# Kernel tuning notes

Measured on AMD Instinct MI355X. Metric: run time of the kernel, lower is better.

The kernel has to match this reference:

```python
import jax, jax.numpy as jnp
import numpy as np

N, D, T = 8192, 512, 65536


def setup_inputs() -> dict:
    key = jax.random.key(0)
    kx, kt = jax.random.split(key)
    x = jax.random.normal(kx, (N, D), dtype=jnp.float32)
    triplets = jax.random.randint(kt, (T, 3), 0, N, dtype=jnp.int64)
    return {"x": x, "triplets": triplets}


def reference(x, triplets):
    # Gather anchor/positive/negative rows instead of building the full NxN
    # distance matrix the torch code materializes; math is identical since
    # dist[i,j] = ||x[i]-x[j]||^2 (clamped at 0, which direct computation guarantees).
    i, j, k = triplets[:, 0], triplets[:, 1], triplets[:, 2]
    xi, xj, xk = x[i], x[j], x[k]          # [T, D] each
    d_ij = jnp.sum((xi - xj) ** 2, axis=-1)  # [T]
    d_ik = jnp.sum((xi - xk) ** 2, axis=-1)  # [T]
    # loss = mean over triplets of log(1 + exp(d_ij - d_ik))
    loss = jnp.mean(jax.nn.softplus(d_ij - d_ik))
    return loss.reshape(1)
```

## Files before the change

### kernel.cpp

```cpp
#include <hip/hip_runtime.h>
#include <hip/hip_fp16.h>


typedef float floatx2 __attribute__((ext_vector_type(2)));

#define NTRIP  65536
#define DIM    512
#define NROWS  8192
#define NSLICE 32
#define SLICE_U4 NROWS
#define GGRP   8
#define TRIP_PER_G (NTRIP / GGRP)
#define BT     1024
#define NIT    (TRIP_PER_G / BT)
#define NSLOT  64
#define SLOT_STRIDE 16

#define XQS_BYTES ((size_t)NSLICE * SLICE_U4 * 16)
#define ZP_BYTES  ((size_t)NSLICE * NTRIP * 2)
#define NEED_NEW  (XQS_BYTES + ZP_BYTES + NSLOT * SLOT_STRIDE * 4 + 64)
#define XQ_BYTES  ((size_t)NROWS * DIM)
#define R7_NBLK   2048
#define NEED_R7   (XQ_BYTES + (size_t)R7_NBLK * 4)

__device__ __forceinline__ float softplus_stable(float z) {
    return fmaxf(z, 0.f) + log1pf(expf(-fabsf(z)));
}

__device__ __forceinline__ unsigned int enc4(float a, float b, float c, float d) {
    unsigned int w = __builtin_amdgcn_cvt_pk_fp8_f32(a, b, 0, false);
    w = __builtin_amdgcn_cvt_pk_fp8_f32(c, d, w, true);
    return w;
}

__device__ __forceinline__ void decode16v(uint4 v, floatx2* f) {
    f[0] = __builtin_amdgcn_cvt_pk_f32_fp8(v.x, false);
    f[1] = __builtin_amdgcn_cvt_pk_f32_fp8(v.x, true);
    f[2] = __builtin_amdgcn_cvt_pk_f32_fp8(v.y, false);
    f[3] = __builtin_amdgcn_cvt_pk_f32_fp8(v.y, true);
    f[4] = __builtin_amdgcn_cvt_pk_f32_fp8(v.z, false);
    f[5] = __builtin_amdgcn_cvt_pk_f32_fp8(v.z, true);
    f[6] = __builtin_amdgcn_cvt_pk_f32_fp8(v.w, false);
    f[7] = __builtin_amdgcn_cvt_pk_f32_fp8(v.w, true);
}

__device__ __forceinline__ void decode4(unsigned int w, float* f) {
    floatx2 p0 = __builtin_amdgcn_cvt_pk_f32_fp8(w, false);
    floatx2 p1 = __builtin_amdgcn_cvt_pk_f32_fp8(w, true);
    f[0] = p0.x; f[1] = p0.y; f[2] = p1.x; f[3] = p1.y;
}

__device__ __forceinline__ void decode16(uint4 v, float* f) {
    decode4(v.x, f);     decode4(v.y, f + 4);
    decode4(v.z, f + 8); decode4(v.w, f + 12);
}


__global__ __launch_bounds__(256) void convert_slice_kernel(
    const float4* __restrict__ x, uint4* __restrict__ xq_s,
    float* __restrict__ slots, unsigned int* __restrict__ counter)
{
    if (blockIdx.x == 0) {
        if (threadIdx.x < NSLOT) slots[threadIdx.x * SLOT_STRIDE] = 0.f;
        if (threadIdx.x == NSLOT) *counter = 0u;
    }
    const int idx = blockIdx.x * 256 + threadIdx.x;
    const int s   = idx >> 13;
    const int r   = idx & (NROWS - 1);
    const float4* src = x + (size_t)r * (DIM / 4) + s * 4;
    float4 a = src[0], b = src[1], c = src[2], d = src[3];
    uint4 o;
    o.x = enc4(a.x, a.y, a.z, a.w);
    o.y = enc4(b.x, b.y, b.z, b.w);
    o.z = enc4(c.x, c.y, c.z, c.w);
    o.w = enc4(d.x, d.y, d.z, d.w);
    xq_s[idx] = o;
}

__global__ __launch_bounds__(BT) void slice_gather_kernel(
    const uint4* __restrict__ xq_s,
    const int*   __restrict__ trip,
    __half*      __restrict__ zph)
{
    __shared__ uint4 sl[SLICE_U4];
    const int s   = blockIdx.x & (NSLICE - 1);
    const int g   = blockIdx.x >> 5;
    const int tid = threadIdx.x;

    const uint4* src = xq_s + (size_t)s * SLICE_U4;
    #pragma unroll
    for (int q = 0; q < SLICE_U4 / BT; ++q)
        sl[tid + q * BT] = src[tid + q * BT];
    __syncthreads();

    __half* zrow = zph + (size_t)s * NTRIP;
    const int tbase = g * TRIP_PER_G + tid;

    int ni = trip[3 * tbase + 0];
    int nj = trip[3 * tbase + 1];
    int nk = trip[3 * tbase + 2];
    int pi = trip[3 * (tbase + BT) + 0];
    int pj = trip[3 * (tbase + BT) + 1];
    int pk = trip[3 * (tbase + BT) + 2];
    uint4 da = sl[ni], db = sl[nj], dc = sl[nk];
    ni = pi; nj = pj; nk = pk;

    #pragma unroll
    for (int it = 0; it < NIT; ++it) {
        pi = 0; pj = 0; pk = 0;
        if (it + 2 < NIT) {
            const int tn = tbase + (it + 2) * BT;
            pi = trip[3 * tn + 0];
            pj = trip[3 * tn + 1];
            pk = trip[3 * tn + 2];
        }
        uint4 ea = {0, 0, 0, 0}, eb = {0, 0, 0, 0}, ec = {0, 0, 0, 0};
        if (it + 1 < NIT) { ea = sl[ni]; eb = sl[nj]; ec = sl[nk]; }
        floatx2 fa[8], fb[8], fc[8];
        decode16v(da, fa); decode16v(db, fb); decode16v(dc, fc);
        floatx2 acc = {0.f, 0.f};
        #pragma unroll
        for (int e = 0; e < 8; ++e) {
            floatx2 d = fa[e] - fb[e];
            floatx2 q = fa[e] - fc[e];
            acc = acc + d * d;
            acc = acc - q * q;
        }
        zrow[tbase + it * BT] = __float2half(acc[0] + acc[1]);
        da = ea; db = eb; dc = ec;
        ni = pi; nj = pj; nk = pk;
    }
}

__global__ __launch_bounds__(256, 4) void combine_kernel(
    const __half* __restrict__ zph,
    float*        __restrict__ slots,
    unsigned int* __restrict__ counter,
    float*        __restrict__ out)
{
    const int tid  = threadIdx.x;
    const int base = (blockIdx.x * 256 + tid) * 4;

    float sp = 0.f;
    #pragma unroll
    for (int p = 0; p < 2; ++p) {
        unsigned int vv[NSLICE];
        #pragma unroll
        for (int s = 0; s < NSLICE; ++s)
            vv[s] = *(const unsigned int*)(zph + (size_t)s * NTRIP
                                           + base + 2 * p);
        float z0 = 0.f, z1 = 0.f;
        #pragma unroll
        for (int s = 0; s < NSLICE; ++s) {
            float2 f = __half22float2(*(__half2*)&vv[s]);
            z0 += f.x; z1 += f.y;
        }
        sp += softplus_stable(z0) + softplus_stable(z1);
    }

    #pragma unroll
    for (int m = 1; m < 64; m <<= 1)
        sp += __shfl_xor(sp, m, 64);

    __shared__ float ws[256 / 64];
    if ((tid & 63) == 0) ws[tid >> 6] = sp;
    __syncthreads();

    __shared__ bool amlast;
    if (tid == 0) {
        float bs = (ws[0] + ws[1]) + (ws[2] + ws[3]);
        atomicAdd(&slots[blockIdx.x * SLOT_STRIDE], bs);
        unsigned int prev = __hip_atomic_fetch_add(
            counter, 1u, __ATOMIC_ACQ_REL, __HIP_MEMORY_SCOPE_AGENT);
        amlast = (prev == 63);
    }
    __syncthreads();

    if (amlast && tid < NSLOT) {
        float v = __hip_atomic_load(&slots[tid * SLOT_STRIDE],
                                    __ATOMIC_RELAXED, __HIP_MEMORY_SCOPE_AGENT);
        #pragma unroll
        for (int m = 1; m < NSLOT; m <<= 1)
            v += __shfl_xor(v, m, 64);
        if (tid == 0) out[0] = v / (float)NTRIP;
    }
}


__global__ __launch_bounds__(256) void convert8_row_kernel(
    const float4* __restrict__ x, uint4* __restrict__ xq)
{
    const int idx = blockIdx.x * 256 + threadIdx.x;
    float4 a = x[(size_t)idx * 4 + 0];
    float4 b = x[(size_t)idx * 4 + 1];
    float4 c = x[(size_t)idx * 4 + 2];
    float4 d = x[(size_t)idx * 4 + 3];
    uint4 o;
    o.x = enc4(a.x, a.y, a.z, a.w);
    o.y = enc4(b.x, b.y, b.z, b.w);
    o.z = enc4(c.x, c.y, c.z, c.w);
    o.w = enc4(d.x, d.y, d.z, d.w);
    xq[idx] = o;
}

__global__ __launch_bounds__(256, 4) void gather8_kernel(
    const uint4* __restrict__ xq,
    const int*   __restrict__ trip,
    float*       __restrict__ partials)
{
    const int lane = threadIdx.x & 63;
    const int half = lane >> 5;
    const int l5   = lane & 31;
    const int wib  = threadIdx.x >> 6;
    const int t0   = (blockIdx.x * 4 + wib) * 8;

    const int4* tp = (const int4*)(trip + 3 * t0);
    int4 w0 = tp[0], w1 = tp[1], w2 = tp[2];
    int4 w3 = tp[3], w4 = tp[4], w5 = tp[5];
    const int id[24] = { w0.x, w0.y, w0.z, w0.w, w1.x, w1.y, w1.z, w1.w,
                         w2.x, w2.y, w2.z, w2.w, w3.x, w3.y, w3.z, w3.w,
                         w4.x, w4.y, w4.z, w4.w, w5.x, w5.y, w5.z, w5.w };

    uint4 r[4][3];
    #pragma unroll
    for (int g = 0; g < 4; ++g) {
        #pragma unroll
        for (int m = 0; m < 3; ++m) {
            const int row = half ? id[3 * (2 * g + 1) + m]
                                 : id[3 * (2 * g) + m];
            r[g][m] = xq[(size_t)row * 32 + l5];
        }
    }

    float z[4] = {0.f, 0.f, 0.f, 0.f};
    #pragma unroll
    for (int g = 0; g < 4; ++g) {
        float fa[16], fb[16], fc[16];
        decode16(r[g][0], fa);
        decode16(r[g][1], fb);
        decode16(r[g][2], fc);
        #pragma unroll
        for (int e = 0; e < 16; ++e) {
            float d = fa[e] - fb[e];
            float q = fa[e] - fc[e];
            z[g] += d * d - q * q;
        }
    }

    #pragma unroll
    for (int m = 1; m <= 16; m <<= 1) {
        #pragma unroll
        for (int g = 0; g < 4; ++g)
            z[g] += __shfl_xor(z[g], m, 64);
    }

    float sp = (softplus_stable(z[0]) + softplus_stable(z[1])) +
               (softplus_stable(z[2]) + softplus_stable(z[3]));
    sp += __shfl_xor(sp, 32, 64);

    __shared__ float wsum[4];
    if (lane == 0) wsum[wib] = sp;
    __syncthreads();
    if (threadIdx.x == 0)
        partials[blockIdx.x] = (wsum[0] + wsum[1]) + (wsum[2] + wsum[3]);
}

__global__ __launch_bounds__(1024) void reduce_kernel(
    const float* __restrict__ partials, float* __restrict__ out, int n)
{
    float s = 0.f;
    for (int idx = threadIdx.x; idx < n; idx += 1024)
        s += partials[idx];
    #pragma unroll
    for (int m = 1; m < 64; m <<= 1)
        s += __shfl_xor(s, m, 64);
    __shared__ float lds[1024 / 64];
    if ((threadIdx.x & 63) == 0) lds[threadIdx.x >> 6] = s;
    __syncthreads();
    if (threadIdx.x == 0) {
        float tot = 0.f;
        #pragma unroll
        for (int q = 0; q < 1024 / 64; ++q) tot += lds[q];
        out[0] = tot / (float)NTRIP;
    }
}

__global__ __launch_bounds__(256) void triplet_partial_f32(
    const float* __restrict__ x,
    const int*   __restrict__ trip,
    float*       __restrict__ partials)
{
    const int lane = threadIdx.x & 63;
    const int wib  = threadIdx.x >> 6;
    const int t    = blockIdx.x * 4 + wib;
    const int i = trip[3 * t + 0];
    const int j = trip[3 * t + 1];
    const int k = trip[3 * t + 2];
    const float4* pi = (const float4*)(x + (size_t)i * DIM) + lane * 2;
    const float4* pj = (const float4*)(x + (size_t)j * DIM) + lane * 2;
    const float4* pk = (const float4*)(x + (size_t)k * DIM) + lane * 2;
    float4 a0 = pi[0], a1 = pi[1];
    float4 b0 = pj[0], b1 = pj[1];
    float4 c0 = pk[0], c1 = pk[1];
    float z = 0.f;
    {
        float d;
        d = a0.x-b0.x; z += d*d; d = a0.y-b0.y; z += d*d;
        d = a0.z-b0.z; z += d*d; d = a0.w-b0.w; z += d*d;
        d = a1.x-b1.x; z += d*d; d = a1.y-b1.y; z += d*d;
        d = a1.z-b1.z; z += d*d; d = a1.w-b1.w; z += d*d;
        d = a0.x-c0.x; z -= d*d; d = a0.y-c0.y; z -= d*d;
        d = a0.z-c0.z; z -= d*d; d = a0.w-c0.w; z -= d*d;
        d = a1.x-c1.x; z -= d*d; d = a1.y-c1.y; z -= d*d;
        d = a1.z-c1.z; z -= d*d; d = a1.w-c1.w; z -= d*d;
    }
    #pragma unroll
    for (int m = 1; m < 64; m <<= 1) z += __shfl_xor(z, m, 64);
    __shared__ float wsum[4];
    if (lane == 0) wsum[wib] = softplus_stable(z);
    __syncthreads();
    if (threadIdx.x == 0)
        partials[blockIdx.x] = (wsum[0] + wsum[1]) + (wsum[2] + wsum[3]);
}

extern "C" void kernel_launch(void* const* d_in, const int* in_sizes, int n_in,
                              void* d_out, int out_size, void* d_ws, size_t ws_size,
                              hipStream_t stream) {
    const float* x    = (const float*)d_in[0];
    const int*   trip = (const int*)d_in[1];
    float*       out  = (float*)d_out;

    if (ws_size >= NEED_NEW) {
        uint4*        xq_s    = (uint4*)d_ws;
        __half*       zph     = (__half*)((char*)d_ws + XQS_BYTES);
        float*        slots   = (float*)((char*)d_ws + XQS_BYTES + ZP_BYTES);
        unsigned int* counter = (unsigned int*)((char*)d_ws + XQS_BYTES
                                 + ZP_BYTES + NSLOT * SLOT_STRIDE * 4);
        convert_slice_kernel<<<(NROWS * NSLICE) / 256, 256, 0, stream>>>(
            (const float4*)x, xq_s, slots, counter);
        slice_gather_kernel<<<NSLICE * GGRP, BT, 0, stream>>>(xq_s, trip, zph);
        combine_kernel<<<NSLOT, 256, 0, stream>>>(zph, slots, counter, out);
    } else if (ws_size >= NEED_R7) {
        uint4* xq       = (uint4*)d_ws;
        float* partials = (float*)((char*)d_ws + XQ_BYTES);
        convert8_row_kernel<<<(NROWS * DIM / 16) / 256, 256, 0, stream>>>(
            (const float4*)x, xq);
        gather8_kernel<<<R7_NBLK, 256, 0, stream>>>(xq, trip, partials);
        reduce_kernel<<<1, 1024, 0, stream>>>(partials, out, R7_NBLK);
    } else {
        float* partials = (float*)d_ws;
        triplet_partial_f32<<<NTRIP / 4, 256, 0, stream>>>(x, trip, partials);
        reduce_kernel<<<1, 1024, 0, stream>>>(partials, out, NTRIP / 4);
    }
}
```

Baseline: 24.34 us.

## Fuse convert, slice-gather and combine into one persistent kernel with grid barriers

Merges the three launches (fp8 slice conversion, per-slice gather, combine/softplus reduction) into a single 256-block kernel of 1024 threads, separated by software grid barriers built on atomic counters. A hipMemsetAsync zeroes the slots and counters before launch. The aim is to remove inter-kernel launch gaps and tail effects. In exchange it relies on all 256 blocks being co-resident for the spin barriers, adds a memset call, and the combine phase uses only 128 of 1024 threads per block.

```diff
diff --git a/kernel.cpp b/kernel.cpp
--- a/kernel.cpp
+++ b/kernel.cpp
@@ -13,12 +13,14 @@
 #define TRIP_PER_G (NTRIP / GGRP)
 #define BT     1024
 #define NIT    (TRIP_PER_G / BT)
-#define NSLOT  64
+#define NBLKF  256
 #define SLOT_STRIDE 16
 
 #define XQS_BYTES ((size_t)NSLICE * SLICE_U4 * 16)
 #define ZP_BYTES  ((size_t)NSLICE * NTRIP * 2)
-#define NEED_NEW  (XQS_BYTES + ZP_BYTES + NSLOT * SLOT_STRIDE * 4 + 64)
+#define SLOTS_BYTES ((size_t)NBLKF * SLOT_STRIDE * 4)
+#define CTR_BYTES 256
+#define NEED_NEW  (XQS_BYTES + ZP_BYTES + SLOTS_BYTES + CTR_BYTES)
 #define XQ_BYTES  ((size_t)NROWS * DIM)
 #define R7_NBLK   2048
 #define NEED_R7   (XQ_BYTES + (size_t)R7_NBLK * 4)
@@ -55,134 +57,145 @@
     decode4(v.z, f + 8); decode4(v.w, f + 12);
 }
 
-
-__global__ __launch_bounds__(256) void convert_slice_kernel(
-    const float4* __restrict__ x, uint4* __restrict__ xq_s,
-    float* __restrict__ slots, unsigned int* __restrict__ counter)
-{
-    if (blockIdx.x == 0) {
-        if (threadIdx.x < NSLOT) slots[threadIdx.x * SLOT_STRIDE] = 0.f;
-        if (threadIdx.x == NSLOT) *counter = 0u;
-    }
-    const int idx = blockIdx.x * 256 + threadIdx.x;
-    const int s   = idx >> 13;
-    const int r   = idx & (NROWS - 1);
-    const float4* src = x + (size_t)r * (DIM / 4) + s * 4;
-    float4 a = src[0], b = src[1], c = src[2], d = src[3];
-    uint4 o;
-    o.x = enc4(a.x, a.y, a.z, a.w);
-    o.y = enc4(b.x, b.y, b.z, b.w);
-    o.z = enc4(c.x, c.y, c.z, c.w);
-    o.w = enc4(d.x, d.y, d.z, d.w);
-    xq_s[idx] = o;
-}
-
-__global__ __launch_bounds__(BT) void slice_gather_kernel(
-    const uint4* __restrict__ xq_s,
-    const int*   __restrict__ trip,
-    __half*      __restrict__ zph)
+__device__ __forceinline__ void grid_barrier(unsigned int* c) {
+    __syncthreads();
+    if (threadIdx.x == 0) {
+        __threadfence();
+        __hip_atomic_fetch_add(c, 1u, __ATOMIC_ACQ_REL,
+                               __HIP_MEMORY_SCOPE_AGENT);
+        while (__hip_atomic_load(c, __ATOMIC_ACQUIRE,
+                                 __HIP_MEMORY_SCOPE_AGENT) < NBLKF) {}
+    }
+    __syncthreads();
+}
+
+
+__global__ __launch_bounds__(BT) void fused_kernel(
+    const float4* __restrict__ x,
+    const int*    __restrict__ trip,
+    uint4*        __restrict__ xq_s,
+    __half*       __restrict__ zph,
+    float*        __restrict__ slots,
+    unsigned int* __restrict__ counters,
+    float*        __restrict__ out)
 {
     __shared__ uint4 sl[SLICE_U4];
-    const int s   = blockIdx.x & (NSLICE - 1);
-    const int g   = blockIdx.x >> 5;
     const int tid = threadIdx.x;
-
-    const uint4* src = xq_s + (size_t)s * SLICE_U4;
-    #pragma unroll
-    for (int q = 0; q < SLICE_U4 / BT; ++q)
-        sl[tid + q * BT] = src[tid + q * BT];
-    __syncthreads();
-
-    __half* zrow = zph + (size_t)s * NTRIP;
-    const int tbase = g * TRIP_PER_G + tid;
-
-    int ni = trip[3 * tbase + 0];
-    int nj = trip[3 * tbase + 1];
-    int nk = trip[3 * tbase + 2];
-    int pi = trip[3 * (tbase + BT) + 0];
-    int pj = trip[3 * (tbase + BT) + 1];
-    int pk = trip[3 * (tbase + BT) + 2];
-    uint4 da = sl[ni], db = sl[nj], dc = sl[nk];
-    ni = pi; nj = pj; nk = pk;
-
-    #pragma unroll
-    for (int it = 0; it < NIT; ++it) {
-        pi = 0; pj = 0; pk = 0;
-        if (it + 2 < NIT) {
-            const int tn = tbase + (it + 2) * BT;
-            pi = trip[3 * tn + 0];
-            pj = trip[3 * tn + 1];
-            pk = trip[3 * tn + 2];
-        }
-        uint4 ea = {0, 0, 0, 0}, eb = {0, 0, 0, 0}, ec = {0, 0, 0, 0};
-        if (it + 1 < NIT) { ea = sl[ni]; eb = sl[nj]; ec = sl[nk]; }
-        floatx2 fa[8], fb[8], fc[8];
-        decode16v(da, fa); decode16v(db, fb); decode16v(dc, fc);
-        floatx2 acc = {0.f, 0.f};
-        #pragma unroll
-        for (int e = 0; e < 8; ++e) {
-            floatx2 d = fa[e] - fb[e];
-            floatx2 q = fa[e] - fc[e];
-            acc = acc + d * d;
-            acc = acc - q * q;
-        }
-        zrow[tbase + it * BT] = __float2half(acc[0] + acc[1]);
-        da = ea; db = eb; dc = ec;
+    const int b   = blockIdx.x;
+
+    {
+        const int idx = b * BT + tid;
+        const int s   = idx >> 13;
+        const int r   = idx & (NROWS - 1);
+        const float4* src = x + (size_t)r * (DIM / 4) + s * 4;
+        float4 a = src[0], bb = src[1], c = src[2], d = src[3];
+        uint4 o;
+        o.x = enc4(a.x, a.y, a.z, a.w);
+        o.y = enc4(bb.x, bb.y, bb.z, bb.w);
+        o.z = enc4(c.x, c.y, c.z, c.w);
+        o.w = enc4(d.x, d.y, d.z, d.w);
+        xq_s[idx] = o;
+    }
+    grid_barrier(&counters[0]);
+
+    {
+        const int s = b & (NSLICE - 1);
+        const int g = b >> 5;
+
+        const uint4* src = xq_s + (size_t)s * SLICE_U4;
+        #pragma unroll
+        for (int q = 0; q < SLICE_U4 / BT; ++q)
+            sl[tid + q * BT] = src[tid + q * BT];
+        __syncthreads();
+
+        __half* zrow = zph + (size_t)s * NTRIP;
+        const int tbase = g * TRIP_PER_G + tid;
+
+        int ni = trip[3 * tbase + 0];
+        int nj = trip[3 * tbase + 1];
+        int nk = trip[3 * tbase + 2];
+        int pi = trip[3 * (tbase + BT) + 0];
+        int pj = trip[3 * (tbase + BT) + 1];
+        int pk = trip[3 * (tbase + BT) + 2];
+        uint4 da = sl[ni], db = sl[nj], dc = sl[nk];
         ni = pi; nj = pj; nk = pk;
-    }
-}
-
-__global__ __launch_bounds__(256, 4) void combine_kernel(
-    const __half* __restrict__ zph,
-    float*        __restrict__ slots,
-    unsigned int* __restrict__ counter,
-    float*        __restrict__ out)
-{
-    const int tid  = threadIdx.x;
-    const int base = (blockIdx.x * 256 + tid) * 4;
-
-    float sp = 0.f;
-    #pragma unroll
-    for (int p = 0; p < 2; ++p) {
-        unsigned int vv[NSLICE];
-        #pragma unroll
-        for (int s = 0; s < NSLICE; ++s)
-            vv[s] = *(const unsigned int*)(zph + (size_t)s * NTRIP
-                                           + base + 2 * p);
-        float z0 = 0.f, z1 = 0.f;
-        #pragma unroll
-        for (int s = 0; s < NSLICE; ++s) {
-            float2 f = __half22float2(*(__half2*)&vv[s]);
-            z0 += f.x; z1 += f.y;
-        }
-        sp += softplus_stable(z0) + softplus_stable(z1);
-    }
-
-    #pragma unroll
-    for (int m = 1; m < 64; m <<= 1)
-        sp += __shfl_xor(sp, m, 64);
-
-    __shared__ float ws[256 / 64];
-    if ((tid & 63) == 0) ws[tid >> 6] = sp;
-    __syncthreads();
-
-    __shared__ bool amlast;
-    if (tid == 0) {
-        float bs = (ws[0] + ws[1]) + (ws[2] + ws[3]);
-        atomicAdd(&slots[blockIdx.x * SLOT_STRIDE], bs);
-        unsigned int prev = __hip_atomic_fetch_add(
-            counter, 1u, __ATOMIC_ACQ_REL, __HIP_MEMORY_SCOPE_AGENT);
-        amlast = (prev == 63);
-    }
-    __syncthreads();
-
-    if (amlast && tid < NSLOT) {
-        float v = __hip_atomic_load(&slots[tid * SLOT_STRIDE],
-                                    __ATOMIC_RELAXED, __HIP_MEMORY_SCOPE_AGENT);
-        #pragma unroll
-        for (int m = 1; m < NSLOT; m <<= 1)
-            v += __shfl_xor(v, m, 64);
-        if (tid == 0) out[0] = v / (float)NTRIP;
+
+        #pragma unroll
+        for (int it = 0; it < NIT; ++it) {
+            pi = 0; pj = 0; pk = 0;
+            if (it + 2 < NIT) {
+                const int tn = tbase + (it + 2) * BT;
+                pi = trip[3 * tn + 0];
+                pj = trip[3 * tn + 1];
+                pk = trip[3 * tn + 2];
+            }
+            uint4 ea = {0,0,0,0}, eb = {0,0,0,0}, ec = {0,0,0,0};
+            if (it + 1 < NIT) { ea = sl[ni]; eb = sl[nj]; ec = sl[nk]; }
+            floatx2 fa[8], fb[8], fc[8];
+            decode16v(da, fa); decode16v(db, fb); decode16v(dc, fc);
+            floatx2 acc = {0.f, 0.f};
+            #pragma unroll
+            for (int e = 0; e < 8; ++e) {
+                floatx2 d = fa[e] - fb[e];
+                floatx2 q = fa[e] - fc[e];
+                acc = acc + d * d;
+                acc = acc - q * q;
+            }
+            zrow[tbase + it * BT] = __float2half(acc[0] + acc[1]);
+            da = ea; db = eb; dc = ec;
+            ni = pi; nj = pj; nk = pk;
+        }
+    }
+    grid_barrier(&counters[16]);
+
+    float* cws = (float*)sl;
+    {
+        float sp = 0.f;
+        if (tid < 128) {
+            const int base = (b * 128 + tid) * 2;
+            unsigned int vv[NSLICE];
+            #pragma unroll
+            for (int s = 0; s < NSLICE; ++s)
+                vv[s] = *(const unsigned int*)(zph + (size_t)s * NTRIP + base);
+            float z0 = 0.f, z1 = 0.f;
+            #pragma unroll
+            for (int s = 0; s < NSLICE; ++s) {
+                float2 f = __half22float2(*(__half2*)&vv[s]);
+                z0 += f.x; z1 += f.y;
+            }
+            sp = softplus_stable(z0) + softplus_stable(z1);
+        }
+        #pragma unroll
+        for (int m = 1; m < 64; m <<= 1)
+            sp += __shfl_xor(sp, m, 64);
+
+        if ((tid & 63) == 0) cws[tid >> 6] = sp;
+        __syncthreads();
+
+        __shared__ bool amlast;
+        if (tid == 0) {
+            float bs = cws[0] + cws[1];
+            atomicAdd(&slots[b * SLOT_STRIDE], bs);
+            unsigned int prev = __hip_atomic_fetch_add(
+                &counters[32], 1u, __ATOMIC_ACQ_REL, __HIP_MEMORY_SCOPE_AGENT);
+            amlast = (prev == NBLKF - 1);
+        }
+        __syncthreads();
+
+        if (amlast) {
+            float v = 0.f;
+            if (tid < NBLKF)
+                v = __hip_atomic_load(&slots[tid * SLOT_STRIDE],
+                                      __ATOMIC_RELAXED, __HIP_MEMORY_SCOPE_AGENT);
+            #pragma unroll
+            for (int m = 1; m < 64; m <<= 1)
+                v += __shfl_xor(v, m, 64);
+            if (tid < NBLKF && (tid & 63) == 0) cws[tid >> 6] = v;
+            __syncthreads();
+            if (tid == 0)
+                out[0] = ((cws[0] + cws[1]) + (cws[2] + cws[3]))
+                         / (float)NTRIP;
+        }
     }
 }
 
@@ -334,12 +347,11 @@
         uint4*        xq_s    = (uint4*)d_ws;
         __half*       zph     = (__half*)((char*)d_ws + XQS_BYTES);
         float*        slots   = (float*)((char*)d_ws + XQS_BYTES + ZP_BYTES);
-        unsigned int* counter = (unsigned int*)((char*)d_ws + XQS_BYTES
-                                 + ZP_BYTES + NSLOT * SLOT_STRIDE * 4);
-        convert_slice_kernel<<<(NROWS * NSLICE) / 256, 256, 0, stream>>>(
-            (const float4*)x, xq_s, slots, counter);
-        slice_gather_kernel<<<NSLICE * GGRP, BT, 0, stream>>>(xq_s, trip, zph);
-        combine_kernel<<<NSLOT, 256, 0, stream>>>(zph, slots, counter, out);
+        unsigned int* counters = (unsigned int*)((char*)d_ws + XQS_BYTES
+                                  + ZP_BYTES + SLOTS_BYTES);
+        hipMemsetAsync(slots, 0, SLOTS_BYTES + CTR_BYTES, stream);
+        fused_kernel<<<NBLKF, BT, 0, stream>>>(
+            (const float4*)x, trip, xq_s, zph, slots, counters, out);
     } else if (ws_size >= NEED_R7) {
         uint4* xq       = (uint4*)d_ws;
         float* partials = (float*)((char*)d_ws + XQ_BYTES);
```

Result: slower. 74.40 us (+205.7%).
